# Optimization experiments

Hardware: AMD Instinct MI355X
Metric: run time of the kernel (lower is better)

## Reference

```python
import jax, jax.numpy as jnp
import numpy as np

# init_kwargs: zs (sorted list of supported atomic numbers)
ZS = jnp.array([0, 1, 6, 7, 8, 11, 13, 14, 16, 17, 26, 29, 47, 78, 79, 83], dtype=jnp.float32)

N_ATOMS = 8_000_000


def setup_inputs() -> dict:
    key = jax.random.key(0)
    # integer-valued atomic numbers in [0, 83); float dtype so gradients exist
    z = jax.random.randint(key, (N_ATOMS,), 0, 83).astype(jnp.float32)
    return {"atomic_numbers": z}


def reference(atomic_numbers):
    K = ZS.shape[0]
    # first index j with ZS[j] >= z (vectorized replacement of the python loop)
    j = jnp.clip(jnp.searchsorted(ZS, atomic_numbers, side="left"), 0, K - 1)
    z_hi = ZS[j]
    exact = z_hi == atomic_numbers           # one-hot branch: z in zs
    j_lo = jnp.clip(j - 1, 0, K - 1)
    z_lo = ZS[j_lo]
    denom = jnp.where(exact, 1.0, z_hi - z_lo)   # safe divide when j_lo == j
    w_hi = jnp.where(exact, 1.0, (atomic_numbers - z_lo) / denom)
    w_lo = jnp.where(exact, 0.0, (z_hi - atomic_numbers) / denom)
    # fused one-hot/interpolation write: [N, K]
    encoded = (w_hi[:, None] * jax.nn.one_hot(j, K, dtype=jnp.float32)
               + w_lo[:, None] * jax.nn.one_hot(j_lo, K, dtype=jnp.float32))
    return encoded
```

## Files before the change

### kernel.cpp

```cpp
#include <hip/hip_runtime.h>


#define K_TAB 16
#define N_Z   83
#define CHUNK 1024
#define BLOCK 256
#define INNER (CHUNK * 4 / BLOCK)

typedef float v4f __attribute__((ext_vector_type(4)));

__global__ __launch_bounds__(BLOCK) void node_encode_kernel(
    const float* __restrict__ z_in,
    float* __restrict__ out,
    int n_atoms, int n_chunks)
{
    __shared__ float lut[N_Z][K_TAB];
    __shared__ float zbuf[CHUNK];

    const int tid = threadIdx.x;

    constexpr float tab[K_TAB] = {0.f, 1.f, 6.f, 7.f, 8.f, 11.f, 13.f, 14.f,
                                  16.f, 17.f, 26.f, 29.f, 47.f, 78.f, 79.f, 83.f};
    if (tid < N_Z) {
        const float zf = (float)tid;
        int j = 0;
        float zlo = tab[0];
        float zhi = tab[K_TAB - 1];
#pragma unroll
        for (int k = 0; k < K_TAB; ++k) {
            const bool lt = (tab[k] < zf);
            j += lt ? 1 : 0;
            zlo = lt ? tab[k] : zlo;
        }
#pragma unroll
        for (int k = K_TAB - 2; k >= 0; --k) {
            zhi = (tab[k] >= zf) ? tab[k] : zhi;
        }
        const bool exact = (zhi == zf);
        const float denom = exact ? 1.f : (zhi - zlo);
        const float inv   = 1.f / denom;
        const float whi   = exact ? 1.f : (zf - zlo) * inv;
        const float wlo   = exact ? 0.f : (zhi - zf) * inv;
        int jl = j - (exact ? 0 : 1);
        if (jl < 0) jl = 0;
#pragma unroll
        for (int c = 0; c < K_TAB; ++c) {
            lut[tid][c] = (c == j ? whi : 0.f) + (c == jl ? wlo : 0.f);
        }
    }

    v4f* __restrict__ out4 = reinterpret_cast<v4f*>(out);
    const int total4 = n_atoms * 4;

    int c = blockIdx.x;
    v4f zreg = {0.f, 0.f, 0.f, 0.f};
    if (c < n_chunks) {
        const int a0 = c * CHUNK + tid * 4;
        if (a0 + 3 < n_atoms) {
            zreg = *reinterpret_cast<const v4f*>(&z_in[a0]);
        } else {
#pragma unroll
            for (int e = 0; e < 4; ++e)
                if (a0 + e < n_atoms) zreg[e] = z_in[a0 + e];
        }
    }

    for (; c < n_chunks; c += gridDim.x) {
        __syncthreads();
        *reinterpret_cast<v4f*>(&zbuf[tid * 4]) = zreg;

        const int cn = c + gridDim.x;
        if (cn < n_chunks) {
            const int a0 = cn * CHUNK + tid * 4;
            if (a0 + 3 < n_atoms) {
                zreg = *reinterpret_cast<const v4f*>(&z_in[a0]);
            } else {
                v4f zt = {0.f, 0.f, 0.f, 0.f};
#pragma unroll
                for (int e = 0; e < 4; ++e)
                    if (a0 + e < n_atoms) zt[e] = z_in[a0 + e];
                zreg = zt;
            }
        }
        __syncthreads();

        const int base4 = c * (CHUNK * 4);
        if (base4 + CHUNK * 4 <= total4) {
#pragma unroll
            for (int k = 0; k < INNER; ++k) {
                const int u  = k * BLOCK + tid;
                const int zi = (int)zbuf[u >> 2];
                const v4f v  = *reinterpret_cast<const v4f*>(&lut[zi][(u & 3) << 2]);
                out4[base4 + u] = v;
            }
        } else {
            for (int k = 0; k < INNER; ++k) {
                const int u = k * BLOCK + tid;
                const int g = base4 + u;
                if (g < total4) {
                    const int zi = (int)zbuf[u >> 2];
                    out4[g] = *reinterpret_cast<const v4f*>(&lut[zi][(u & 3) << 2]);
                }
            }
        }
    }
}

extern "C" void kernel_launch(void* const* d_in, const int* in_sizes, int n_in,
                              void* d_out, int out_size, void* d_ws, size_t ws_size,
                              hipStream_t stream) {
    const float* z = (const float*)d_in[0];
    float* out = (float*)d_out;
    const int n_atoms = in_sizes[0];

    const int n_chunks = (n_atoms + CHUNK - 1) / CHUNK;
    const int grid = 2048;

    node_encode_kernel<<<grid, BLOCK, 0, stream>>>(z, out, n_atoms, n_chunks);
}
```

Before: 109.6 us.

## Double-buffer z staging with LDS-only barriers, one barrier per chunk

```diff
diff --git a/kernel.cpp b/kernel.cpp
--- a/kernel.cpp
+++ b/kernel.cpp
@@ -9,13 +9,33 @@
 
 typedef float v4f __attribute__((ext_vector_type(4)));
 
+__device__ __forceinline__ void lds_only_barrier() {
+    __asm__ volatile("s_waitcnt lgkmcnt(0)" ::: "memory");
+    __builtin_amdgcn_s_barrier();
+    __builtin_amdgcn_sched_barrier(0);
+}
+
+__device__ __forceinline__ v4f load_chunk_z(const float* __restrict__ z_in,
+                                            int c, int tid, int n_atoms) {
+    const int a0 = c * CHUNK + tid * 4;
+    v4f r = {0.f, 0.f, 0.f, 0.f};
+    if (a0 + 3 < n_atoms) {
+        r = *reinterpret_cast<const v4f*>(&z_in[a0]);
+    } else {
+#pragma unroll
+        for (int e = 0; e < 4; ++e)
+            if (a0 + e < n_atoms) r[e] = z_in[a0 + e];
+    }
+    return r;
+}
+
 __global__ __launch_bounds__(BLOCK) void node_encode_kernel(
     const float* __restrict__ z_in,
     float* __restrict__ out,
     int n_atoms, int n_chunks)
 {
     __shared__ float lut[N_Z][K_TAB];
-    __shared__ float zbuf[CHUNK];
+    __shared__ float zbuf[2][CHUNK];
 
     const int tid = threadIdx.x;
 
@@ -53,43 +73,26 @@
     const int total4 = n_atoms * 4;
 
     int c = blockIdx.x;
-    v4f zreg = {0.f, 0.f, 0.f, 0.f};
     if (c < n_chunks) {
-        const int a0 = c * CHUNK + tid * 4;
-        if (a0 + 3 < n_atoms) {
-            zreg = *reinterpret_cast<const v4f*>(&z_in[a0]);
-        } else {
-#pragma unroll
-            for (int e = 0; e < 4; ++e)
-                if (a0 + e < n_atoms) zreg[e] = z_in[a0 + e];
-        }
+        const v4f z0 = load_chunk_z(z_in, c, tid, n_atoms);
+        *reinterpret_cast<v4f*>(&zbuf[0][tid * 4]) = z0;
     }
+    lds_only_barrier();
 
-    for (; c < n_chunks; c += gridDim.x) {
-        __syncthreads();
-        *reinterpret_cast<v4f*>(&zbuf[tid * 4]) = zreg;
+    int p = 0;
+    for (; c < n_chunks; c += gridDim.x, ++p) {
+        const int cn = c + gridDim.x;
+        const bool haveN = (cn < n_chunks);
+        v4f zregN = {0.f, 0.f, 0.f, 0.f};
+        if (haveN) zregN = load_chunk_z(z_in, cn, tid, n_atoms);
 
-        const int cn = c + gridDim.x;
-        if (cn < n_chunks) {
-            const int a0 = cn * CHUNK + tid * 4;
-            if (a0 + 3 < n_atoms) {
-                zreg = *reinterpret_cast<const v4f*>(&z_in[a0]);
-            } else {
-                v4f zt = {0.f, 0.f, 0.f, 0.f};
-#pragma unroll
-                for (int e = 0; e < 4; ++e)
-                    if (a0 + e < n_atoms) zt[e] = z_in[a0 + e];
-                zreg = zt;
-            }
-        }
-        __syncthreads();
-
+        const float* __restrict__ zb = zbuf[p & 1];
         const int base4 = c * (CHUNK * 4);
         if (base4 + CHUNK * 4 <= total4) {
 #pragma unroll
             for (int k = 0; k < INNER; ++k) {
                 const int u  = k * BLOCK + tid;
-                const int zi = (int)zbuf[u >> 2];
+                const int zi = (int)zb[u >> 2];
                 const v4f v  = *reinterpret_cast<const v4f*>(&lut[zi][(u & 3) << 2]);
                 out4[base4 + u] = v;
             }
@@ -98,11 +101,16 @@
                 const int u = k * BLOCK + tid;
                 const int g = base4 + u;
                 if (g < total4) {
-                    const int zi = (int)zbuf[u >> 2];
+                    const int zi = (int)zb[u >> 2];
                     out4[g] = *reinterpret_cast<const v4f*>(&lut[zi][(u & 3) << 2]);
                 }
             }
         }
+
+        if (haveN) {
+            *reinterpret_cast<v4f*>(&zbuf[(p + 1) & 1][tid * 4]) = zregN;
+        }
+        lds_only_barrier();
     }
 }
 
@@ -114,7 +122,9 @@
     const int n_atoms = in_sizes[0];
 
     const int n_chunks = (n_atoms + CHUNK - 1) / CHUNK;
-    const int grid = 2048;
+    const int phases   = 4;
+    int grid = (n_chunks + phases - 1) / phases;
+    if (grid > 2048) grid = 2048;
 
     node_encode_kernel<<<grid, BLOCK, 0, stream>>>(z, out, n_atoms, n_chunks);
 }
```

After: 110.2 us. About the same (+0.6%).

## Use single-wave blocks with double-buffered LDS to drop block barriers

Applied to the files above, without the earlier changes.

```diff
diff --git a/kernel.cpp b/kernel.cpp
--- a/kernel.cpp
+++ b/kernel.cpp
@@ -3,26 +3,26 @@
 
 #define K_TAB 16
 #define N_Z   83
-#define CHUNK 1024
-#define BLOCK 256
-#define INNER (CHUNK * 4 / BLOCK)
+#define WSZ   64
+#define CA    256
+#define INNER (CA / 16)
 
 typedef float v4f __attribute__((ext_vector_type(4)));
 
-__global__ __launch_bounds__(BLOCK) void node_encode_kernel(
+__global__ __launch_bounds__(WSZ) void node_encode_kernel(
     const float* __restrict__ z_in,
     float* __restrict__ out,
     int n_atoms, int n_chunks)
 {
     __shared__ float lut[N_Z][K_TAB];
-    __shared__ float zbuf[CHUNK];
+    __shared__ float zl[2][CA];
 
-    const int tid = threadIdx.x;
+    const int lane = threadIdx.x;
 
     constexpr float tab[K_TAB] = {0.f, 1.f, 6.f, 7.f, 8.f, 11.f, 13.f, 14.f,
                                   16.f, 17.f, 26.f, 29.f, 47.f, 78.f, 79.f, 83.f};
-    if (tid < N_Z) {
-        const float zf = (float)tid;
+    for (int row = lane; row < N_Z; row += WSZ) {
+        const float zf = (float)row;
         int j = 0;
         float zlo = tab[0];
         float zhi = tab[K_TAB - 1];
@@ -45,17 +45,18 @@
         if (jl < 0) jl = 0;
 #pragma unroll
         for (int c = 0; c < K_TAB; ++c) {
-            lut[tid][c] = (c == j ? whi : 0.f) + (c == jl ? wlo : 0.f);
+            lut[row][c] = (c == j ? whi : 0.f) + (c == jl ? wlo : 0.f);
         }
     }
 
     v4f* __restrict__ out4 = reinterpret_cast<v4f*>(out);
-    const int total4 = n_atoms * 4;
+    const int nwaves = gridDim.x;
+    const int gwave  = blockIdx.x;
 
-    int c = blockIdx.x;
+    int c = gwave;
     v4f zreg = {0.f, 0.f, 0.f, 0.f};
     if (c < n_chunks) {
-        const int a0 = c * CHUNK + tid * 4;
+        const int a0 = c * CA + lane * 4;
         if (a0 + 3 < n_atoms) {
             zreg = *reinterpret_cast<const v4f*>(&z_in[a0]);
         } else {
@@ -65,13 +66,13 @@
         }
     }
 
-    for (; c < n_chunks; c += gridDim.x) {
-        __syncthreads();
-        *reinterpret_cast<v4f*>(&zbuf[tid * 4]) = zreg;
+    int p = 0;
+    for (; c < n_chunks; c += nwaves, ++p) {
+        *reinterpret_cast<v4f*>(&zl[p & 1][lane * 4]) = zreg;
 
-        const int cn = c + gridDim.x;
+        const int cn = c + nwaves;
         if (cn < n_chunks) {
-            const int a0 = cn * CHUNK + tid * 4;
+            const int a0 = cn * CA + lane * 4;
             if (a0 + 3 < n_atoms) {
                 zreg = *reinterpret_cast<const v4f*>(&z_in[a0]);
             } else {
@@ -82,23 +83,24 @@
                 zreg = zt;
             }
         }
-        __syncthreads();
 
-        const int base4 = c * (CHUNK * 4);
-        if (base4 + CHUNK * 4 <= total4) {
+        const float* __restrict__ zb = zl[p & 1];
+        const long base4 = (long)c * (CA * 4);
+        if ((c + 1) * CA <= n_atoms) {
 #pragma unroll
             for (int k = 0; k < INNER; ++k) {
-                const int u  = k * BLOCK + tid;
-                const int zi = (int)zbuf[u >> 2];
+                const int u  = k * WSZ + lane;
+                const int zi = (int)zb[u >> 2];
                 const v4f v  = *reinterpret_cast<const v4f*>(&lut[zi][(u & 3) << 2]);
                 out4[base4 + u] = v;
             }
         } else {
+            const long total4 = (long)n_atoms * 4;
             for (int k = 0; k < INNER; ++k) {
-                const int u = k * BLOCK + tid;
-                const int g = base4 + u;
+                const int u = k * WSZ + lane;
+                const long g = base4 + u;
                 if (g < total4) {
-                    const int zi = (int)zbuf[u >> 2];
+                    const int zi = (int)zb[u >> 2];
                     out4[g] = *reinterpret_cast<const v4f*>(&lut[zi][(u & 3) << 2]);
                 }
             }
@@ -113,8 +115,8 @@
     float* out = (float*)d_out;
     const int n_atoms = in_sizes[0];
 
-    const int n_chunks = (n_atoms + CHUNK - 1) / CHUNK;
-    const int grid = 2048;
+    const int n_chunks = (n_atoms + CA - 1) / CA;
+    const int grid = 1024;
 
-    node_encode_kernel<<<grid, BLOCK, 0, stream>>>(z, out, n_atoms, n_chunks);
+    node_encode_kernel<<<grid, WSZ, 0, stream>>>(z, out, n_atoms, n_chunks);
 }
```

Result: faster. 105.0 us (-4.2%).
